# Kernel optimization log

Measured on AMD Instinct MI355X. Metric: run time of the kernel, lower is better.

## Reference

```python
import jax, jax.numpy as jnp
import numpy as np

M = 262144          # rows of A == prod(out_shape) == 512*512
N = 262144          # cols of A == prod(x.shape)
NNZ = 8388608       # 32 nonzeros per row on average
OUT_SHAPE = (512, 512)


def setup_inputs() -> dict:
    key = jax.random.key(0)
    k1, k2, k3, k4 = jax.random.split(key, 4)
    A_rows = jax.random.randint(k1, (NNZ,), 0, M, dtype=jnp.int32)
    A_cols = jax.random.randint(k2, (NNZ,), 0, N, dtype=jnp.int32)
    A_vals = jax.random.normal(k3, (NNZ,), dtype=jnp.float32)
    x = jax.random.normal(k4, OUT_SHAPE, dtype=jnp.float32)
    return {"x": x, "A_vals": A_vals, "A_rows": A_rows, "A_cols": A_cols}


def reference(x, A_vals, A_rows, A_cols):
    # x.reshape(A.shape[1], 1); torch.sparse.mm(A, x); reshape(out_shape)
    xf = x.reshape(-1)                                   # [N]
    contrib = A_vals * jnp.take(xf, A_cols)              # [NNZ] gather + multiply
    y = jax.ops.segment_sum(contrib, A_rows, num_segments=M)  # scatter-add over rows
    return y.reshape(OUT_SHAPE).astype(jnp.float32)
```

## Files before the change

### kernel.cpp

```cpp
#include <hip/hip_runtime.h>


#define BINS_MAXB   64
#define ROW_SHIFT   13
#define ROWS_PER_BIN 8192
#define ENT         4096
#define SLICES      16


__global__ __launch_bounds__(256) void zero_out_kernel(float* __restrict__ y, int n) {
    int i = blockIdx.x * blockDim.x + threadIdx.x;
    if (i < n) y[i] = 0.0f;
}

__global__ __launch_bounds__(256) void spmv_coo_scatter(
    const float* __restrict__ vals, const int* __restrict__ rows,
    const int* __restrict__ cols, const float* __restrict__ x,
    float* __restrict__ y, int nnz)
{
    int i = (blockIdx.x * blockDim.x + threadIdx.x) * 4;
    if (i + 3 < nnz) {
        float4 v = *reinterpret_cast<const float4*>(vals + i);
        int4   r = *reinterpret_cast<const int4*>(rows + i);
        int4   c = *reinterpret_cast<const int4*>(cols + i);
        atomicAdd(&y[r.x], v.x * x[c.x]);
        atomicAdd(&y[r.y], v.y * x[c.y]);
        atomicAdd(&y[r.z], v.z * x[c.z]);
        atomicAdd(&y[r.w], v.w * x[c.w]);
    } else {
        for (; i < nnz; ++i) atomicAdd(&y[rows[i]], vals[i] * x[cols[i]]);
    }
}


__global__ __launch_bounds__(64) void init_cursors(unsigned* __restrict__ gcur, int bins) {
    int t = threadIdx.x;
    if (t < bins) gcur[t] = 0u;
}

__global__ __launch_bounds__(256) void scatter2_kernel(
    const int*   __restrict__ rows, const int* __restrict__ cols,
    const float* __restrict__ vals, const float* __restrict__ x, int nnz,
    unsigned* __restrict__ gcur, unsigned cap,
    unsigned short* __restrict__ okeys, float* __restrict__ ocontrib, int bins)
{
    __shared__ unsigned cnt[BINS_MAXB], lstart[BINS_MAXB], sresv[BINS_MAXB];
    __shared__ int dstb[BINS_MAXB];
    __shared__ unsigned cur2[BINS_MAXB];
    __shared__ unsigned total_s;
    __shared__ unsigned short skey[ENT];
    __shared__ float          sval[ENT];
    __shared__ unsigned char  sbin[ENT];

    const int t = threadIdx.x;
    for (int i = t; i < bins; i += 256) cnt[i] = 0u;
    __syncthreads();

    const int seg = blockIdx.x * ENT;

    int   rr[16];
    float ff[16];

    #pragma unroll
    for (int ch = 0; ch < 4; ++ch) {
        int base = seg + ch * 1024 + t * 4;
        if (base + 3 < nnz) {
            int4   r4 = *reinterpret_cast<const int4*>(rows + base);
            int4   c4 = *reinterpret_cast<const int4*>(cols + base);
            float4 v4 = *reinterpret_cast<const float4*>(vals + base);
            rr[ch*4+0] = r4.x; ff[ch*4+0] = v4.x * x[c4.x];
            rr[ch*4+1] = r4.y; ff[ch*4+1] = v4.y * x[c4.y];
            rr[ch*4+2] = r4.z; ff[ch*4+2] = v4.z * x[c4.z];
            rr[ch*4+3] = r4.w; ff[ch*4+3] = v4.w * x[c4.w];
        } else {
            #pragma unroll
            for (int j = 0; j < 4; ++j) {
                int idx = base + j;
                if (idx < nnz) { rr[ch*4+j] = rows[idx]; ff[ch*4+j] = vals[idx] * x[cols[idx]]; }
                else           { rr[ch*4+j] = -1; ff[ch*4+j] = 0.0f; }
            }
        }
    }
    #pragma unroll
    for (int j = 0; j < 16; ++j)
        if (rr[j] >= 0) atomicAdd(&cnt[rr[j] >> ROW_SHIFT], 1u);
    __syncthreads();

    if (t < bins) sresv[t] = atomicAdd(&gcur[t], cnt[t]);
    if (t == 0) {
        unsigned run = 0;
        for (int b = 0; b < bins; ++b) { lstart[b] = run; run += cnt[b]; }
        total_s = run;
    }
    __syncthreads();
    if (t < bins) {
        dstb[t] = (int)sresv[t] - (int)lstart[t];
        cur2[t] = lstart[t];
    }
    __syncthreads();

    #pragma unroll
    for (int j = 0; j < 16; ++j) {
        if (rr[j] >= 0) {
            int b = rr[j] >> ROW_SHIFT;
            unsigned p = atomicAdd(&cur2[b], 1u);
            skey[p] = (unsigned short)(rr[j] & (ROWS_PER_BIN - 1));
            sval[p] = ff[j];
            sbin[p] = (unsigned char)b;
        }
    }
    __syncthreads();

    const unsigned total = total_s;
    for (unsigned i = t; i < total; i += 256) {
        int b = sbin[i];
        unsigned off = (unsigned)(dstb[b] + (int)i);
        if (off < cap) {
            size_t dst = (size_t)b * cap + off;
            okeys[dst]    = skey[i];
            ocontrib[dst] = sval[i];
        }
    }
}

__global__ __launch_bounds__(256) void accum2_kernel(
    const unsigned short* __restrict__ okeys, const float* __restrict__ ocontrib,
    const unsigned* __restrict__ gcur, unsigned cap,
    float* __restrict__ partials)
{
    __shared__ float acc[ROWS_PER_BIN];
    const int t = threadIdx.x;
    const int bin = blockIdx.x / SLICES;
    const int sl  = blockIdx.x % SLICES;

    #pragma unroll
    for (int i = 0; i < ROWS_PER_BIN / 256; ++i) acc[t + i * 256] = 0.0f;
    __syncthreads();

    unsigned count = gcur[bin];
    if (count > cap) count = cap;
    unsigned chunk = (count + SLICES - 1) / SLICES;
    chunk = (chunk + 3u) & ~3u;
    unsigned lo = (unsigned)sl * chunk;
    unsigned hi = lo + chunk; if (hi > count) hi = count;

    const unsigned short* k = okeys    + (size_t)bin * cap;
    const float*          c = ocontrib + (size_t)bin * cap;

    unsigned i = lo + (unsigned)t * 4u;
    for (; i + 3u < hi; i += 1024u) {
        ushort4 k4 = *reinterpret_cast<const ushort4*>(k + i);
        float4  c4 = *reinterpret_cast<const float4*>(c + i);
        atomicAdd(&acc[k4.x], c4.x);
        atomicAdd(&acc[k4.y], c4.y);
        atomicAdd(&acc[k4.z], c4.z);
        atomicAdd(&acc[k4.w], c4.w);
    }
    for (; i < hi; ++i) atomicAdd(&acc[k[i]], c[i]);
    __syncthreads();

    float* p = partials + (size_t)blockIdx.x * ROWS_PER_BIN;
    #pragma unroll
    for (int j = 0; j < ROWS_PER_BIN / 1024; ++j) {
        int l = j * 1024 + t * 4;
        *reinterpret_cast<float4*>(p + l) = *reinterpret_cast<const float4*>(&acc[l]);
    }
}

__global__ __launch_bounds__(256) void reduce2_kernel(
    const float* __restrict__ partials, float* __restrict__ y, int out_size)
{
    int r = blockIdx.x * 256 + threadIdx.x;
    if (r >= out_size) return;
    int bin = r >> ROW_SHIFT;
    int local = r & (ROWS_PER_BIN - 1);
    const float* p = partials + ((size_t)bin * SLICES) * ROWS_PER_BIN + local;
    float s = 0.0f;
    #pragma unroll
    for (int j = 0; j < SLICES; ++j) s += p[(size_t)j * ROWS_PER_BIN];
    y[r] = s;
}

extern "C" void kernel_launch(void* const* d_in, const int* in_sizes, int n_in,
                              void* d_out, int out_size, void* d_ws, size_t ws_size,
                              hipStream_t stream) {
    const float* x    = (const float*)d_in[0];
    const float* vals = (const float*)d_in[1];
    const int*   rows = (const int*)d_in[2];
    const int*   cols = (const int*)d_in[3];
    float* y = (float*)d_out;

    const int nnz  = in_sizes[1];
    const int bins = (out_size + ROWS_PER_BIN - 1) / ROWS_PER_BIN;
    const int nb   = (nnz + ENT - 1) / ENT;
    unsigned cap = (unsigned)(nnz / (bins > 0 ? bins : 1)) + 16384u;
    cap = (cap + 3u) & ~3u;

    auto align256 = [](size_t v) { return (v + 255) & ~(size_t)255; };
    size_t off_contrib  = 0;
    size_t off_keys     = align256(off_contrib + (size_t)bins * cap * 4);
    size_t off_partials = align256(off_keys + (size_t)bins * cap * 2);
    size_t off_gcur     = align256(off_partials + (size_t)bins * SLICES * ROWS_PER_BIN * 4);
    size_t need         = align256(off_gcur + (size_t)bins * 4);

    const bool ok = (bins >= 1) && (bins <= BINS_MAXB) && (need <= ws_size) && (nnz > 0);

    if (!ok) {
        zero_out_kernel<<<(out_size + 255) / 256, 256, 0, stream>>>(y, out_size);
        spmv_coo_scatter<<<(nnz + 1023) / 1024, 256, 0, stream>>>(vals, rows, cols, x, y, nnz);
        return;
    }

    char* w = (char*)d_ws;
    float*          ocontrib = (float*)(w + off_contrib);
    unsigned short* okeys    = (unsigned short*)(w + off_keys);
    float*          partials = (float*)(w + off_partials);
    unsigned*       gcur     = (unsigned*)(w + off_gcur);

    init_cursors<<<1, 64, 0, stream>>>(gcur, bins);
    scatter2_kernel<<<nb, 256, 0, stream>>>(rows, cols, vals, x, nnz, gcur, cap,
                                            okeys, ocontrib, bins);
    accum2_kernel<<<bins * SLICES, 256, 0, stream>>>(okeys, ocontrib, gcur, cap, partials);
    reduce2_kernel<<<(out_size + 255) / 256, 256, 0, stream>>>(partials, y, out_size);
}
```

Measured before the change: 232.0 us.

## Specialize binning to fixed 32 bins, pad cursors, batch gathers, widen accum and reduce

Hardcodes 32 bins and replaces the serial per-block prefix with a wave shuffle scan. Global bin cursors are padded to separate cache lines to cut atomic contention. The column gathers of x are batched after all index loads so more memory requests are in flight. The accumulation kernel moves to 512 threads with 4x unrolled loads, and the reduce kernel is vectorized to float4. In exchange the fast path now only handles outputs of exactly 32*8192 rows.

```diff
diff --git a/kernel.cpp b/kernel.cpp
--- a/kernel.cpp
+++ b/kernel.cpp
@@ -1,11 +1,15 @@
 #include <hip/hip_runtime.h>
 
 
-#define BINS_MAXB   64
-#define ROW_SHIFT   13
+#define BINS         32
+#define ROW_SHIFT    13
 #define ROWS_PER_BIN 8192
-#define ENT         4096
-#define SLICES      16
+#define ENT          4096
+#define CUR_STRIDE   32
+#define SLICES       16
+
+typedef int   __attribute__((ext_vector_type(4))) i32x4;
+typedef float __attribute__((ext_vector_type(4))) f32x4;
 
 
 __global__ __launch_bounds__(256) void zero_out_kernel(float* __restrict__ y, int n) {
@@ -33,69 +37,81 @@
 }
 
 
-__global__ __launch_bounds__(64) void init_cursors(unsigned* __restrict__ gcur, int bins) {
-    int t = threadIdx.x;
-    if (t < bins) gcur[t] = 0u;
+__global__ __launch_bounds__(256) void init_cursors(unsigned* __restrict__ gcur, int n) {
+    int i = blockIdx.x * 256 + threadIdx.x;
+    if (i < n) gcur[i] = 0u;
 }
 
 __global__ __launch_bounds__(256) void scatter2_kernel(
     const int*   __restrict__ rows, const int* __restrict__ cols,
     const float* __restrict__ vals, const float* __restrict__ x, int nnz,
     unsigned* __restrict__ gcur, unsigned cap,
-    unsigned short* __restrict__ okeys, float* __restrict__ ocontrib, int bins)
-{
-    __shared__ unsigned cnt[BINS_MAXB], lstart[BINS_MAXB], sresv[BINS_MAXB];
-    __shared__ int dstb[BINS_MAXB];
-    __shared__ unsigned cur2[BINS_MAXB];
+    unsigned short* __restrict__ okeys, float* __restrict__ ocontrib)
+{
+    __shared__ unsigned cnt[BINS];
+    __shared__ int      dstb[BINS];
+    __shared__ unsigned cur2[BINS];
     __shared__ unsigned total_s;
     __shared__ unsigned short skey[ENT];
     __shared__ float          sval[ENT];
     __shared__ unsigned char  sbin[ENT];
 
     const int t = threadIdx.x;
-    for (int i = t; i < bins; i += 256) cnt[i] = 0u;
+    if (t < BINS) cnt[t] = 0u;
     __syncthreads();
 
     const int seg = blockIdx.x * ENT;
 
     int   rr[16];
+    int   cc[16];
     float ff[16];
 
-    #pragma unroll
-    for (int ch = 0; ch < 4; ++ch) {
-        int base = seg + ch * 1024 + t * 4;
-        if (base + 3 < nnz) {
-            int4   r4 = *reinterpret_cast<const int4*>(rows + base);
-            int4   c4 = *reinterpret_cast<const int4*>(cols + base);
-            float4 v4 = *reinterpret_cast<const float4*>(vals + base);
-            rr[ch*4+0] = r4.x; ff[ch*4+0] = v4.x * x[c4.x];
-            rr[ch*4+1] = r4.y; ff[ch*4+1] = v4.y * x[c4.y];
-            rr[ch*4+2] = r4.z; ff[ch*4+2] = v4.z * x[c4.z];
-            rr[ch*4+3] = r4.w; ff[ch*4+3] = v4.w * x[c4.w];
-        } else {
+    if (seg + ENT <= nnz) {
+        #pragma unroll
+        for (int ch = 0; ch < 4; ++ch) {
+            int base = seg + ch * 1024 + t * 4;
+            i32x4 r4 = *reinterpret_cast<const i32x4*>(rows + base);
+            i32x4 c4 = *reinterpret_cast<const i32x4*>(cols + base);
+            f32x4 v4 = *reinterpret_cast<const f32x4*>(vals + base);
+            rr[ch*4+0] = r4.x; cc[ch*4+0] = c4.x; ff[ch*4+0] = v4.x;
+            rr[ch*4+1] = r4.y; cc[ch*4+1] = c4.y; ff[ch*4+1] = v4.y;
+            rr[ch*4+2] = r4.z; cc[ch*4+2] = c4.z; ff[ch*4+2] = v4.z;
+            rr[ch*4+3] = r4.w; cc[ch*4+3] = c4.w; ff[ch*4+3] = v4.w;
+        }
+        #pragma unroll
+        for (int j = 0; j < 16; ++j) ff[j] *= x[cc[j]];
+    } else {
+        #pragma unroll
+        for (int ch = 0; ch < 4; ++ch) {
             #pragma unroll
             for (int j = 0; j < 4; ++j) {
-                int idx = base + j;
-                if (idx < nnz) { rr[ch*4+j] = rows[idx]; ff[ch*4+j] = vals[idx] * x[cols[idx]]; }
-                else           { rr[ch*4+j] = -1; ff[ch*4+j] = 0.0f; }
+                int idx = seg + ch * 1024 + t * 4 + j;
+                if (idx < nnz) { rr[ch*4+j] = rows[idx]; cc[ch*4+j] = cols[idx]; ff[ch*4+j] = vals[idx]; }
+                else           { rr[ch*4+j] = -1; cc[ch*4+j] = 0; ff[ch*4+j] = 0.0f; }
             }
         }
-    }
+        #pragma unroll
+        for (int j = 0; j < 16; ++j) if (rr[j] >= 0) ff[j] *= x[cc[j]];
+    }
+
     #pragma unroll
     for (int j = 0; j < 16; ++j)
         if (rr[j] >= 0) atomicAdd(&cnt[rr[j] >> ROW_SHIFT], 1u);
     __syncthreads();
 
-    if (t < bins) sresv[t] = atomicAdd(&gcur[t], cnt[t]);
-    if (t == 0) {
-        unsigned run = 0;
-        for (int b = 0; b < bins; ++b) { lstart[b] = run; run += cnt[b]; }
-        total_s = run;
-    }
-    __syncthreads();
-    if (t < bins) {
-        dstb[t] = (int)sresv[t] - (int)lstart[t];
-        cur2[t] = lstart[t];
+    if (t < BINS) {
+        unsigned c = cnt[t];
+        unsigned resv = atomicAdd(&gcur[t * CUR_STRIDE], c);
+        unsigned v = c;
+        #pragma unroll
+        for (int d = 1; d < BINS; d <<= 1) {
+            unsigned o = __shfl_up(v, d, 64);
+            if (t >= d) v += o;
+        }
+        unsigned ls = v - c;
+        cur2[t] = ls;
+        dstb[t] = (int)resv - (int)ls;
+        if (t == BINS - 1) total_s = v;
     }
     __syncthreads();
 
@@ -123,24 +139,25 @@
     }
 }
 
-__global__ __launch_bounds__(256) void accum2_kernel(
+__global__ __launch_bounds__(512) void accum2_kernel(
     const unsigned short* __restrict__ okeys, const float* __restrict__ ocontrib,
     const unsigned* __restrict__ gcur, unsigned cap,
     float* __restrict__ partials)
 {
     __shared__ float acc[ROWS_PER_BIN];
-    const int t = threadIdx.x;
+    const int t   = threadIdx.x;
     const int bin = blockIdx.x / SLICES;
-    const int sl  = blockIdx.x % SLICES;
-
-    #pragma unroll
-    for (int i = 0; i < ROWS_PER_BIN / 256; ++i) acc[t + i * 256] = 0.0f;
-    __syncthreads();
-
-    unsigned count = gcur[bin];
+    const int sl  = blockIdx.x - bin * SLICES;
+
+    float4 z = make_float4(0.f, 0.f, 0.f, 0.f);
+    #pragma unroll
+    for (int i = 0; i < ROWS_PER_BIN / (512 * 4); ++i)
+        *reinterpret_cast<float4*>(&acc[(i * 512 + t) * 4]) = z;
+    __syncthreads();
+
+    unsigned count = gcur[bin * CUR_STRIDE];
     if (count > cap) count = cap;
-    unsigned chunk = (count + SLICES - 1) / SLICES;
-    chunk = (chunk + 3u) & ~3u;
+    unsigned chunk = ((count + SLICES - 1u) / SLICES + 3u) & ~3u;
     unsigned lo = (unsigned)sl * chunk;
     unsigned hi = lo + chunk; if (hi > count) hi = count;
 
@@ -148,7 +165,26 @@
     const float*          c = ocontrib + (size_t)bin * cap;
 
     unsigned i = lo + (unsigned)t * 4u;
-    for (; i + 3u < hi; i += 1024u) {
+
+    for (; i + 6147u < hi; i += 8192u) {
+        ushort4 k0 = *reinterpret_cast<const ushort4*>(k + i);
+        ushort4 k1 = *reinterpret_cast<const ushort4*>(k + i + 2048u);
+        ushort4 k2 = *reinterpret_cast<const ushort4*>(k + i + 4096u);
+        ushort4 k3 = *reinterpret_cast<const ushort4*>(k + i + 6144u);
+        float4  c0 = *reinterpret_cast<const float4*>(c + i);
+        float4  c1 = *reinterpret_cast<const float4*>(c + i + 2048u);
+        float4  c2 = *reinterpret_cast<const float4*>(c + i + 4096u);
+        float4  c3 = *reinterpret_cast<const float4*>(c + i + 6144u);
+        atomicAdd(&acc[k0.x], c0.x); atomicAdd(&acc[k0.y], c0.y);
+        atomicAdd(&acc[k0.z], c0.z); atomicAdd(&acc[k0.w], c0.w);
+        atomicAdd(&acc[k1.x], c1.x); atomicAdd(&acc[k1.y], c1.y);
+        atomicAdd(&acc[k1.z], c1.z); atomicAdd(&acc[k1.w], c1.w);
+        atomicAdd(&acc[k2.x], c2.x); atomicAdd(&acc[k2.y], c2.y);
+        atomicAdd(&acc[k2.z], c2.z); atomicAdd(&acc[k2.w], c2.w);
+        atomicAdd(&acc[k3.x], c3.x); atomicAdd(&acc[k3.y], c3.y);
+        atomicAdd(&acc[k3.z], c3.z); atomicAdd(&acc[k3.w], c3.w);
+    }
+    for (; i + 3u < hi; i += 2048u) {
         ushort4 k4 = *reinterpret_cast<const ushort4*>(k + i);
         float4  c4 = *reinterpret_cast<const float4*>(c + i);
         atomicAdd(&acc[k4.x], c4.x);
@@ -161,8 +197,8 @@
 
     float* p = partials + (size_t)blockIdx.x * ROWS_PER_BIN;
     #pragma unroll
-    for (int j = 0; j < ROWS_PER_BIN / 1024; ++j) {
-        int l = j * 1024 + t * 4;
+    for (int i2 = 0; i2 < ROWS_PER_BIN / (512 * 4); ++i2) {
+        int l = (i2 * 512 + t) * 4;
         *reinterpret_cast<float4*>(p + l) = *reinterpret_cast<const float4*>(&acc[l]);
     }
 }
@@ -170,15 +206,17 @@
 __global__ __launch_bounds__(256) void reduce2_kernel(
     const float* __restrict__ partials, float* __restrict__ y, int out_size)
 {
-    int r = blockIdx.x * 256 + threadIdx.x;
-    if (r >= out_size) return;
-    int bin = r >> ROW_SHIFT;
-    int local = r & (ROWS_PER_BIN - 1);
+    int r0 = (blockIdx.x * 256 + threadIdx.x) * 4;
+    if (r0 >= out_size) return;
+    int bin = r0 >> ROW_SHIFT, local = r0 & (ROWS_PER_BIN - 1);
     const float* p = partials + ((size_t)bin * SLICES) * ROWS_PER_BIN + local;
-    float s = 0.0f;
-    #pragma unroll
-    for (int j = 0; j < SLICES; ++j) s += p[(size_t)j * ROWS_PER_BIN];
-    y[r] = s;
+    float4 s = make_float4(0.f, 0.f, 0.f, 0.f);
+    #pragma unroll
+    for (int j = 0; j < SLICES; ++j) {
+        float4 v = *reinterpret_cast<const float4*>(p + (size_t)j * ROWS_PER_BIN);
+        s.x += v.x; s.y += v.y; s.z += v.z; s.w += v.w;
+    }
+    *reinterpret_cast<float4*>(y + r0) = s;
 }
 
 extern "C" void kernel_launch(void* const* d_in, const int* in_sizes, int n_in,
@@ -192,18 +230,20 @@
 
     const int nnz  = in_sizes[1];
     const int bins = (out_size + ROWS_PER_BIN - 1) / ROWS_PER_BIN;
-    const int nb   = (nnz + ENT - 1) / ENT;
+
     unsigned cap = (unsigned)(nnz / (bins > 0 ? bins : 1)) + 16384u;
     cap = (cap + 3u) & ~3u;
 
     auto align256 = [](size_t v) { return (v + 255) & ~(size_t)255; };
+
     size_t off_contrib  = 0;
-    size_t off_keys     = align256(off_contrib + (size_t)bins * cap * 4);
-    size_t off_partials = align256(off_keys + (size_t)bins * cap * 2);
-    size_t off_gcur     = align256(off_partials + (size_t)bins * SLICES * ROWS_PER_BIN * 4);
-    size_t need         = align256(off_gcur + (size_t)bins * 4);
-
-    const bool ok = (bins >= 1) && (bins <= BINS_MAXB) && (need <= ws_size) && (nnz > 0);
+    size_t off_keys     = align256(off_contrib + (size_t)BINS * cap * 4);
+    size_t off_partials = align256(off_keys + (size_t)BINS * cap * 2);
+    size_t off_gcur     = align256(off_partials + (size_t)BINS * SLICES * ROWS_PER_BIN * 4);
+    size_t need         = align256(off_gcur + (size_t)BINS * CUR_STRIDE * 4);
+
+    const bool ok = (bins == BINS) && (need <= ws_size) && (nnz > 0) &&
+                    (out_size == BINS * ROWS_PER_BIN);
 
     if (!ok) {
         zero_out_kernel<<<(out_size + 255) / 256, 256, 0, stream>>>(y, out_size);
@@ -217,9 +257,10 @@
     float*          partials = (float*)(w + off_partials);
     unsigned*       gcur     = (unsigned*)(w + off_gcur);
 
-    init_cursors<<<1, 64, 0, stream>>>(gcur, bins);
-    scatter2_kernel<<<nb, 256, 0, stream>>>(rows, cols, vals, x, nnz, gcur, cap,
-                                            okeys, ocontrib, bins);
-    accum2_kernel<<<bins * SLICES, 256, 0, stream>>>(okeys, ocontrib, gcur, cap, partials);
-    reduce2_kernel<<<(out_size + 255) / 256, 256, 0, stream>>>(partials, y, out_size);
-}
+    const int ncur = BINS * CUR_STRIDE;
+    init_cursors<<<(ncur + 255) / 256, 256, 0, stream>>>(gcur, ncur);
+    scatter2_kernel<<<(nnz + ENT - 1) / ENT, 256, 0, stream>>>(
+        rows, cols, vals, x, nnz, gcur, cap, okeys, ocontrib);
+    accum2_kernel<<<BINS * SLICES, 512, 0, stream>>>(okeys, ocontrib, gcur, cap, partials);
+    reduce2_kernel<<<(out_size / 4 + 255) / 256, 256, 0, stream>>>(partials, y, out_size);
+}
```

Measured after the change: 217.3 us. 6.4% less time.
